# Kernel optimization log

Hardware: AMD Instinct MI355X
Metric: run time of the kernel (lower is better)

## Reference

```python
import jax, jax.numpy as jnp
import numpy as np

EPS = 1e-5  # torch BatchNorm1d default eps


def _bn(x, axes):
    # BatchNorm in training mode with gamma=1, beta=0 (torch init values):
    # normalize with biased batch statistics over the given axes.
    m = x.mean(axes, keepdims=True)
    v = x.var(axes, keepdims=True)
    return (x - m) * jax.lax.rsqrt(v + EPS)


def setup_inputs() -> dict:
    key = jax.random.key(0)
    ks = jax.random.split(key, 12)
    N, M = 50000, 12
    OF, F, E, H = 92, 64, 41, 128
    Z = 2 * F + E  # 169 = concat(node, nbr_node, edge)

    def w(k, shape, fan):
        return jax.random.normal(k, shape, jnp.float32) * np.float32(1.0 / np.sqrt(fan))

    return {
        "node_fea": jax.random.normal(ks[0], (N, OF), jnp.float32),
        "edge_fea": jax.random.uniform(ks[1], (N, M, E), dtype=jnp.float32),
        "nbr_offset": jax.random.randint(ks[2], (N, M, 3), -1, 2).astype(jnp.float32),
        "atom_pos": jax.random.uniform(ks[3], (N, 3), dtype=jnp.float32) * 10.0,
        "cells": jnp.broadcast_to(jnp.eye(3, dtype=jnp.float32) * 10.0, (N, 3, 3))
                 + jax.random.normal(ks[4], (N, 3, 3), jnp.float32) * 0.1,
        "edge_idx": jax.random.randint(ks[5], (N, M), 0, N),
        "W_emb": w(ks[6], (OF, F), OF), "b_emb": jnp.zeros((F,), jnp.float32),
        "W_pre_node": w(ks[7], (3, Z, 2 * F), Z), "b_pre_node": jnp.zeros((3, 2 * F), jnp.float32),
        "W_pre_edge": w(ks[8], (3, Z, 2 * E), Z), "b_pre_edge": jnp.zeros((3, 2 * E), jnp.float32),
        "W_dist": w(ks[9], (Z, H), Z), "b_dist": jnp.zeros((H,), jnp.float32),
        "W_const": w(ks[10], (Z, H), Z), "b_const": jnp.zeros((H,), jnp.float32),
    }


def reference(node_fea, edge_fea, nbr_offset, atom_pos, cells, edge_idx,
              W_emb, b_emb, W_pre_node, b_pre_node, W_pre_edge, b_pre_edge,
              W_dist, b_dist, W_const, b_const):
    N, M = edge_idx.shape
    lrelu = jax.nn.leaky_relu  # torch LeakyReLU default slope 0.01
    sig = jax.nn.sigmoid
    sp = jax.nn.softplus

    # get_distance: neighbor Cartesian positions via unit-cell offsets
    off_cart = jnp.einsum('nmi,nij->nmj', nbr_offset, cells)         # (N,M,3)
    diff = atom_pos[edge_idx] + off_cart - atom_pos[:, None, :]       # (N,M,3)
    distance = jnp.sqrt(jnp.sum(diff * diff, -1, keepdims=True) + 1e-12)  # (N,M,1)

    node = node_fea @ W_emb + b_emb  # embedding -> (N,64)

    for l in range(W_pre_node.shape[0]):  # n_conv = 3 ConvLayers
        nbr = node[edge_idx]  # gather (N,M,F)
        z = jnp.concatenate(
            [jnp.broadcast_to(node[:, None, :], (N, M, node.shape[-1])), nbr, edge_fea],
            axis=2)  # (N,M,169)
        # node branch: linear -> BN -> sigmoid*leakyrelu gate -> sum over M -> BN -> residual
        zn = _bn(z @ W_pre_node[l] + b_pre_node[l], (0, 1))  # (N,M,128)
        nf, nc = jnp.split(zn, 2, axis=2)
        aggr = jnp.sum(sig(nf) * lrelu(nc), axis=1)           # (N,64)
        node = lrelu(node + _bn(aggr, (0,)))
        # edge branch: linear -> BN -> gate -> BN -> residual
        ze = _bn(z @ W_pre_edge[l] + b_pre_edge[l], (0, 1))   # (N,M,82)
        ef, ec = jnp.split(ze, 2, axis=2)
        edge_fea = lrelu(edge_fea + _bn(sig(ef) * lrelu(ec), (0, 1)))

    nbr = node[edge_idx]
    bond_fea = jnp.concatenate(
        [jnp.broadcast_to(node[:, None, :], (N, M, node.shape[-1])), nbr, edge_fea],
        axis=2)  # (N,M,169)

    # n_h_dist == 1 branch: softplus(BN(linear) + distance), mean over channels
    bd = sp(_bn(bond_fea @ W_dist + b_dist, (0, 1)) + distance)
    bd = jnp.mean(bd, axis=2, keepdims=True)                  # (N,M,1)
    # n_h_const == 1 branch: softplus(BN(linear)), mean over channels, / N
    bc = sp(_bn(bond_fea @ W_const + b_const, (0, 1)))
    bc = jnp.mean(bc, axis=2, keepdims=True) / N              # (N,M,1)

    return jnp.concatenate([bd, bc], axis=2)                  # (N,M,2)
```

## Files before the change

kernel.cpp:

```cpp
#include <hip/hip_runtime.h>
#include <math.h>

#define NN 50000
#define MM 12
#define NM 600000
#define OF 92
#define FF 64
#define EE 41
#define ES 48
#define ZZ 169
#define RPB 96
#define NPB 8
#define NTILE 6250
#define NBLK2 3125
#define KP 200
#define KSTEPS 6
#define MT 6
#define NSLICE 64
#define PSTRIDE 1024
#define TPB 512

typedef __bf16 bf16x8 __attribute__((ext_vector_type(8)));
typedef float  f32x4  __attribute__((ext_vector_type(4)));

__device__ __forceinline__ float lrelu(float x){ return fmaxf(x, 0.01f*x); }
__device__ __forceinline__ float sigm(float x){ return __builtin_amdgcn_rcpf(1.f+__expf(-x)); }
__device__ __forceinline__ float softpl(float x){ return fmaxf(x,0.f) + __logf(1.f+__expf(-fabsf(x))); }
__device__ __forceinline__ unsigned short f2bf(float f){
    __bf16 h = (__bf16)f;
    return __builtin_bit_cast(unsigned short, h);
}
__device__ __forceinline__ float b2f(unsigned short u){
    unsigned int b = ((unsigned int)u) << 16;
    return __builtin_bit_cast(float, b);
}

__global__ __launch_bounds__(256) void pack_w(const float* __restrict__ Wn,
    const float* __restrict__ We, const float* __restrict__ Wd,
    const float* __restrict__ Wc, unsigned short* __restrict__ dst)
{
    int idx = blockIdx.x*256 + threadIdx.x;
    if (idx >= 4*49152) return;
    int j    = idx & 7;
    int lane = (idx >> 3) & 63;
    int ntks = (idx >> 9) % 96;
    int L    = idx / 49152;
    int nt = ntks & 15, ks = ntks >> 4;
    int k   = ks*32 + (lane>>4)*8 + j;
    int col = nt*16 + (lane&15);
    float v = 0.f;
    if (k < ZZ) {
        if (L < 3) {
            if (col < 128)                       v = Wn[((size_t)L*ZZ + k)*128 + col];
            else if (col >= 128 && col < 128+EE) v = We[((size_t)L*ZZ + k)*82 + (col-128)];
            else if (col >= 192 && col < 192+EE) v = We[((size_t)L*ZZ + k)*82 + 41 + (col-192)];
        } else {
            if (col < 128) v = Wd[(size_t)k*128 + col];
            else           v = Wc[(size_t)k*128 + (col-128)];
        }
    }
    dst[idx] = f2bf(v);
}

__global__ __launch_bounds__(256) void k_dist(const float* __restrict__ off,
    const float* __restrict__ apos, const float* __restrict__ cells,
    const int* __restrict__ eidx, float* __restrict__ distb)
{
    int idx = blockIdx.x*256 + threadIdx.x;
    if (idx >= NM) return;
    int n = idx / MM;
    const float* o  = off + (size_t)idx*3;
    const float* cl = cells + (size_t)n*9;
    int n2 = eidx[idx];
    float o0=o[0], o1=o[1], o2=o[2];
    float dd = 1e-12f;
    #pragma unroll
    for (int j=0;j<3;j++){
        float oc = o0*cl[0*3+j] + o1*cl[1*3+j] + o2*cl[2*3+j];
        float d = apos[(size_t)n2*3+j] + oc - apos[(size_t)n*3+j];
        dd += d*d;
    }
    distb[idx] = sqrtf(dd);
}

__global__ __launch_bounds__(256) void k_cvt(const float* __restrict__ src,
    unsigned short* __restrict__ e)
{
    int idx = blockIdx.x*256 + threadIdx.x;
    if (idx >= NM*ES) return;
    int gr = idx / ES;
    int c  = idx - gr*ES;
    e[idx] = (c < EE) ? f2bf(src[(size_t)gr*EE + c]) : (unsigned short)0;
}

__global__ __launch_bounds__(256) void k_emb(const float* __restrict__ nf,
    const float* __restrict__ W, const float* __restrict__ b,
    unsigned short* __restrict__ node0)
{
    int idx = blockIdx.x*256 + threadIdx.x;
    if (idx >= NN*FF) return;
    int n = idx >> 6, c = idx & 63;
    float s = b[c];
    for (int k=0;k<OF;k++) s = fmaf(nf[(size_t)n*OF+k], W[k*FF+c], s);
    node0[idx] = f2bf(s);
}

__global__ __launch_bounds__(256) void k_red(float* __restrict__ P,
    float* __restrict__ dst, int lo, int hi)
{
    for (int c = lo + threadIdx.x; c < hi; c += 256) {
        float s = 0.f;
        #pragma unroll 8
        for (int sl = 0; sl < NSLICE; ++sl) s += P[sl*PSTRIDE + c];
        dst[c] = s;
        #pragma unroll 8
        for (int sl = 0; sl < NSLICE; ++sl) P[sl*PSTRIDE + c] = 0.f;
    }
}

__device__ __forceinline__ void stage_load(uint4* __restrict__ R,
    const unsigned short* __restrict__ node_src, const unsigned short* __restrict__ ebuf,
    const unsigned short* __restrict__ gbuf, const int* __restrict__ eidx,
    int n0, int tid, bool upd)
{
    const int gr0 = n0 * MM;
    const int r0 = tid >> 3, ch = tid & 7;
    const bool two = tid < 256;
    const uint4 z4 = make_uint4(0u,0u,0u,0u);
    int e0 = eidx[gr0 + r0];
    R[0] = *(const uint4*)(node_src + (size_t)(n0 + r0/MM)*FF + ch*8);
    R[1] = *(const uint4*)(node_src + (size_t)e0*FF + ch*8);
    R[2] = z4; R[3] = z4; R[4] = z4; R[5] = z4; R[6] = z4; R[7] = z4;
    if (ch < 6) {
        R[2] = *(const uint4*)(ebuf + (size_t)(gr0+r0)*ES + ch*8);
        if (upd) R[3] = *(const uint4*)(gbuf + (size_t)(gr0+r0)*ES + ch*8);
    }
    if (two) {
        int r1 = r0 + 64;
        int e1 = eidx[gr0 + r1];
        R[4] = *(const uint4*)(node_src + (size_t)(n0 + r1/MM)*FF + ch*8);
        R[5] = *(const uint4*)(node_src + (size_t)e1*FF + ch*8);
        if (ch < 6) {
            R[6] = *(const uint4*)(ebuf + (size_t)(gr0+r1)*ES + ch*8);
            if (upd) R[7] = *(const uint4*)(gbuf + (size_t)(gr0+r1)*ES + ch*8);
        }
    }
}

__device__ __forceinline__ uint4 upd_edge8(uint4 e, uint4 g,
    const float* __restrict__ mmv, const float* __restrict__ isv, int ch)
{
    unsigned short es[8], gs[8], os[8];
    *(uint4*)es = e; *(uint4*)gs = g;
    #pragma unroll
    for (int j=0;j<8;j++){
        int c = ch*8+j;
        if (c < EE){
            float v = (b2f(gs[j]) - mmv[j]) * isv[j];
            os[j] = f2bf(lrelu(b2f(es[j]) + v));
        } else os[j] = es[j];
    }
    return *(uint4*)os;
}

__device__ __forceinline__ void stage_write(uint4* __restrict__ R,
    unsigned short* __restrict__ Zl, unsigned short* __restrict__ ebuf_wb,
    int n0, int tid, bool upd,
    const float* __restrict__ mmv, const float* __restrict__ isv)
{
    const int gr0 = n0 * MM;
    const int r0 = tid >> 3, ch = tid & 7;
    const bool two = tid < 256;
    uint4 d0 = R[2];
    if (upd && ch < 6) {
        d0 = upd_edge8(R[2], R[3], mmv, isv, ch);
        *(uint4*)(ebuf_wb + (size_t)(gr0+r0)*ES + ch*8) = d0;
    }
    *(uint4*)(Zl + r0*KP + ch*8)       = R[0];
    *(uint4*)(Zl + r0*KP + 64 + ch*8)  = R[1];
    *(uint4*)(Zl + r0*KP + 128 + ch*8) = d0;
    if (two) {
        int r1 = r0 + 64;
        uint4 d1 = R[6];
        if (upd && ch < 6) {
            d1 = upd_edge8(R[6], R[7], mmv, isv, ch);
            *(uint4*)(ebuf_wb + (size_t)(gr0+r1)*ES + ch*8) = d1;
        }
        *(uint4*)(Zl + r1*KP + ch*8)       = R[4];
        *(uint4*)(Zl + r1*KP + 64 + ch*8)  = R[5];
        *(uint4*)(Zl + r1*KP + 128 + ch*8) = d1;
    }
}

template<bool ZERO>
__device__ __forceinline__ void mfma_core(const unsigned short* __restrict__ Zl,
    const unsigned short* __restrict__ Wpk, int h, int sw, int lane, f32x4 (&acc)[MT][2])
{
    const int quad = lane >> 4, li = lane & 15;
    if (ZERO) {
        #pragma unroll
        for (int mt=0;mt<MT;mt++){
            acc[mt][0] = (f32x4){0.f,0.f,0.f,0.f};
            acc[mt][1] = (f32x4){0.f,0.f,0.f,0.f};
        }
    }
    const int nt0 = h*8 + sw;
    #pragma unroll 2
    for (int ks=0; ks<KSTEPS; ++ks) {
        bf16x8 bfr0 = *(const bf16x8*)(Wpk + (((ks*16 + nt0    )*64 + lane) << 3));
        bf16x8 bfr1 = *(const bf16x8*)(Wpk + (((ks*16 + nt0 + 4)*64 + lane) << 3));
        bf16x8 afr[MT];
        #pragma unroll
        for (int mt=0;mt<MT;mt++)
            afr[mt] = *(const bf16x8*)(Zl + (mt*16+li)*KP + ks*32 + quad*8);
        #pragma unroll
        for (int mt=0;mt<MT;mt++){
            acc[mt][0] = __builtin_amdgcn_mfma_f32_16x16x32_bf16(afr[mt], bfr0, acc[mt][0], 0, 0, 0);
            acc[mt][1] = __builtin_amdgcn_mfma_f32_16x16x32_bf16(afr[mt], bfr1, acc[mt][1], 0, 0, 0);
        }
    }
}

__device__ __forceinline__ void stats_epi(const f32x4 (&acc)[MT][2], int h, int sw, int lane,
    float* __restrict__ Ps)
{
    const int quad = lane>>4, li = lane&15;
    #pragma unroll
    for (int t=0;t<2;t++){
        float s=0.f, q=0.f;
        #pragma unroll
        for (int mt=0;mt<MT;mt++)
            #pragma unroll
            for (int r=0;r<4;r++){ float v = acc[mt][t][r]; s+=v; q = fmaf(v,v,q); }
        s += __shfl_xor(s,16); s += __shfl_xor(s,32);
        q += __shfl_xor(q,16); q += __shfl_xor(q,32);
        if (quad == 0) {
            int col = h*128 + t*64 + sw*16 + li;
            atomicAdd(&Ps[col], s);
            atomicAdd(&Ps[256+col], q);
        }
    }
}

__global__ __launch_bounds__(TPB,3) void k_stats(
    const unsigned short* __restrict__ node_src, unsigned short* __restrict__ ebuf,
    const unsigned short* __restrict__ gbuf, const int* __restrict__ eidx,
    const unsigned short* __restrict__ Wpk,
    const float* __restrict__ gS, const float* __restrict__ gQ,
    float* __restrict__ Pst)
{
    __shared__ unsigned short Zl[RPB*KP];
    const int tid = threadIdx.x, w = tid>>6, lane = tid&63;
    const int h = w>>2, sw = w&3;
    const bool upd = (gS != nullptr);
    const int ch = tid & 7;
    float mmv[8], isv[8];
    if (upd) {
        #pragma unroll
        for (int j=0;j<8;j++){
            int c = ch*8+j;
            float mm = 0.f, is = 0.f;
            if (c < EE) {
                mm = gS[c]*(1.f/(float)NM);
                float vv = gQ[c]*(1.f/(float)NM) - mm*mm;
                is = rsqrtf(vv + 1e-5f);
            }
            mmv[j] = mm; isv[j] = is;
        }
    }
    const int t0 = blockIdx.x * 2;
    uint4 R[8];
    stage_load(R, node_src, ebuf, gbuf, eidx, t0*NPB, tid, upd);
    stage_write(R, Zl, ebuf, t0*NPB, tid, upd, mmv, isv);
    __syncthreads();
    stage_load(R, node_src, ebuf, gbuf, eidx, (t0+1)*NPB, tid, upd);
    f32x4 acc[MT][2];
    mfma_core<true>(Zl, Wpk, h, sw, lane, acc);
    __syncthreads();
    stage_write(R, Zl, ebuf, (t0+1)*NPB, tid, upd, mmv, isv);
    __syncthreads();
    mfma_core<false>(Zl, Wpk, h, sw, lane, acc);
    float* Ps = Pst + (size_t)(blockIdx.x & (NSLICE-1))*PSTRIDE;
    stats_epi(acc, h, sw, lane, Ps);
}

__global__ __launch_bounds__(TPB,3) void k_apply_re(
    const unsigned short* __restrict__ node_src, const unsigned short* __restrict__ ebuf,
    const int* __restrict__ eidx, const unsigned short* __restrict__ Wpk,
    const float* __restrict__ preS, const float* __restrict__ preQ,
    float* __restrict__ aggr, unsigned short* __restrict__ gbuf,
    float* __restrict__ Pst)
{
    __shared__ __align__(16) char smem[RPB*KP*2];
    unsigned short* Zl = (unsigned short*)smem;
    float* gL = (float*)smem;
    const int tid = threadIdx.x, w = tid>>6, lane = tid&63;
    const int quad = lane>>4, li = lane&15;
    const int h = w>>2, sw = w&3;
    const int t0 = blockIdx.x * 2;

    uint4 R[8];
    stage_load(R, node_src, ebuf, nullptr, eidx, t0*NPB, tid, false);
    stage_write(R, Zl, nullptr, t0*NPB, tid, false, nullptr, nullptr);
    __syncthreads();
    stage_load(R, node_src, ebuf, nullptr, eidx, (t0+1)*NPB, tid, false);

    const int cg0 = sw*16 + li;
    float sc[2], bi[2];
    #pragma unroll
    for (int t=0;t<2;t++){
        int col = h*128 + t*64 + cg0;
        float mm = preS[col]*(1.f/(float)NM);
        float vv = preQ[col]*(1.f/(float)NM) - mm*mm;
        float is = rsqrtf(vv + 1e-5f);
        sc[t] = is; bi[t] = -mm*is;
    }
    const bool ce_ok = cg0 < EE;
    float* Ps = Pst + (size_t)(blockIdx.x & (NSLICE-1))*PSTRIDE;
    float pg = 0.f, pq = 0.f;
    float sAcc = 0.f, sQq = 0.f;

    f32x4 acc[MT][2];
    #pragma unroll
    for (int tile=0; tile<2; ++tile){
        const int n0 = (t0+tile)*NPB;
        const int gr0 = n0 * MM;
        mfma_core<true>(Zl, Wpk, h, sw, lane, acc);
        __syncthreads();
        if (h == 0) {
            #pragma unroll
            for (int mt=0;mt<MT;mt++)
                #pragma unroll
                for (int r=0;r<4;r++){
                    int row = mt*16 + quad*4 + r;
                    float nf = fmaf(acc[mt][0][r], sc[0], bi[0]);
                    float nc = fmaf(acc[mt][1][r], sc[1], bi[1]);
                    gL[row*68 + cg0] = sigm(nf) * lrelu(nc);
                }
        } else {
            #pragma unroll
            for (int mt=0;mt<MT;mt++)
                #pragma unroll
                for (int r=0;r<4;r++){
                    int row = mt*16 + quad*4 + r;
                    float ef = fmaf(acc[mt][0][r], sc[0], bi[0]);
                    float ec = fmaf(acc[mt][1][r], sc[1], bi[1]);
                    float gv = sigm(ef)*lrelu(ec);
                    if (ce_ok) {
                        gbuf[(size_t)(gr0+row)*ES + cg0] = f2bf(gv);
                        pg += gv; pq = fmaf(gv,gv,pq);
                    }
                }
        }
        __syncthreads();
        {
            float vsum = 0.f;
            #pragma unroll
            for (int jj=0;jj<MM;jj++) vsum += gL[(w*MM+jj)*68 + lane];
            aggr[(size_t)(n0+w)*64 + lane] = vsum;
            sAcc += vsum; sQq = fmaf(vsum,vsum,sQq);
        }
        if (tile == 0) {
            __syncthreads();
            stage_write(R, Zl, nullptr, (t0+1)*NPB, tid, false, nullptr, nullptr);
            __syncthreads();
        }
    }
    pg += __shfl_xor(pg,16); pg += __shfl_xor(pg,32);
    pq += __shfl_xor(pq,16); pq += __shfl_xor(pq,32);
    if (h==1 && quad==0 && ce_ok){ atomicAdd(&Ps[640+cg0], pg); atomicAdd(&Ps[704+cg0], pq); }
    atomicAdd(&Ps[512+lane], sAcc);
    atomicAdd(&Ps[576+lane], sQq);
}

__global__ __launch_bounds__(256) void k_upd_node(const unsigned short* __restrict__ cur,
    const float* __restrict__ aggr, const float* __restrict__ aS,
    const float* __restrict__ aQ, unsigned short* __restrict__ nxt)
{
    int idx = blockIdx.x*256 + threadIdx.x;
    if (idx >= NN*8) return;
    int n = idx >> 3, ch = idx & 7;
    int base = n*64 + ch*8;
    float4 a0 = *(const float4*)(aggr + base);
    float4 a1 = *(const float4*)(aggr + base + 4);
    uint4 cu = *(const uint4*)(cur + base);
    unsigned short cs[8]; *(uint4*)cs = cu;
    float av[8] = {a0.x,a0.y,a0.z,a0.w,a1.x,a1.y,a1.z,a1.w};
    unsigned short os[8];
    #pragma unroll
    for (int j=0;j<8;j++){
        int c = ch*8+j;
        float mm = aS[c]*(1.f/(float)NN);
        float vv = aQ[c]*(1.f/(float)NN) - mm*mm;
        float is = rsqrtf(vv + 1e-5f);
        float v = (av[j] - mm) * is;
        os[j] = f2bf(lrelu(b2f(cs[j]) + v));
    }
    *(uint4*)(nxt + base) = *(uint4*)os;
}

__global__ __launch_bounds__(TPB,3) void k_final_re(
    const unsigned short* __restrict__ node_src, const unsigned short* __restrict__ ebuf,
    const int* __restrict__ eidx, const unsigned short* __restrict__ Wpk,
    const float* __restrict__ fS, const float* __restrict__ fQ,
    const float* __restrict__ distb, float* __restrict__ out)
{
    __shared__ __align__(16) char smem[RPB*KP*2];
    unsigned short* Zl = (unsigned short*)smem;
    float* bufD = (float*)smem;
    float* bufC = (float*)(smem + 8192);
    const int tid = threadIdx.x, w = tid>>6, lane = tid&63;
    const int quad = lane>>4, li = lane&15;
    const int h = w>>2, sw = w&3;
    const int t0 = blockIdx.x * 2;

    uint4 R[8];
    stage_load(R, node_src, ebuf, nullptr, eidx, t0*NPB, tid, false);
    stage_write(R, Zl, nullptr, t0*NPB, tid, false, nullptr, nullptr);
    __syncthreads();
    stage_load(R, node_src, ebuf, nullptr, eidx, (t0+1)*NPB, tid, false);

    const int cg0 = sw*16 + li;
    float sc[2], bi[2];
    #pragma unroll
    for (int t=0;t<2;t++){
        int col = h*128 + t*64 + cg0;
        float mm = fS[col]*(1.f/(float)NM);
        float vv = fQ[col]*(1.f/(float)NM) - mm*mm;
        float is = rsqrtf(vv + 1e-5f);
        sc[t] = is; bi[t] = -mm*is;
    }
    const int liq = li >> 2;
    const bool wr = (li & 3) == 0;

    f32x4 acc[MT][2];
    #pragma unroll
    for (int tile=0; tile<2; ++tile){
        const int n0 = (t0+tile)*NPB;
        const int gr0 = n0 * MM;
        mfma_core<true>(Zl, Wpk, h, sw, lane, acc);
        __syncthreads();
        float* buf = (h == 0) ? bufD : bufC;
        #pragma unroll
        for (int mt=0;mt<MT;mt++)
            #pragma unroll
            for (int r=0;r<4;r++){
                int row = mt*16 + quad*4 + r;
                float v0 = fmaf(acc[mt][0][r], sc[0], bi[0]);
                float v1 = fmaf(acc[mt][1][r], sc[1], bi[1]);
                float p;
                if (h == 0) {
                    float dv = distb[gr0 + row];
                    p = softpl(v0 + dv) + softpl(v1 + dv);
                } else {
                    p = softpl(v0) + softpl(v1);
                }
                p += __shfl_xor(p,1); p += __shfl_xor(p,2);
                if (wr) buf[row*17 + sw*4 + liq] = p;
            }
        __syncthreads();
        if (tid < 2*RPB) {
            int hh = tid >= RPB;
            int row = tid - (hh ? RPB : 0);
            const float* bsrc = hh ? bufC : bufD;
            float s = 0.f;
            #pragma unroll
            for (int t=0;t<16;t++) s += bsrc[row*17+t];
            size_t gr = gr0 + row;
            out[gr*2 + hh] = hh ? s * (1.f/128.f) * (1.f/(float)NN) : s * (1.f/128.f);
        }
        if (tile == 0) {
            __syncthreads();
            stage_write(R, Zl, nullptr, (t0+1)*NPB, tid, false, nullptr, nullptr);
            __syncthreads();
        }
    }
}

extern "C" void kernel_launch(void* const* d_in, const int* in_sizes, int n_in,
                              void* d_out, int out_size, void* d_ws, size_t ws_size,
                              hipStream_t stream)
{
    const float* node_fea = (const float*)d_in[0];
    const float* edge_in  = (const float*)d_in[1];
    const float* nbr_off  = (const float*)d_in[2];
    const float* apos     = (const float*)d_in[3];
    const float* cells    = (const float*)d_in[4];
    const int*   eidx     = (const int*)  d_in[5];
    const float* W_emb    = (const float*)d_in[6];
    const float* b_emb    = (const float*)d_in[7];
    const float* W_pn     = (const float*)d_in[8];
    const float* W_pe     = (const float*)d_in[10];
    const float* W_dist   = (const float*)d_in[12];
    const float* W_cst    = (const float*)d_in[14];
    float* out = (float*)d_out;
    char* ws = (char*)d_ws;

    size_t o = 0;
    auto alloc = [&](size_t bytes) { char* p = ws + o; o += (bytes + 255) & ~(size_t)255; return p; };
    unsigned short* node0 = (unsigned short*)alloc((size_t)NN*FF*2);
    unsigned short* node1 = (unsigned short*)alloc((size_t)NN*FF*2);
    unsigned short* ebuf  = (unsigned short*)alloc((size_t)NM*ES*2);
    unsigned short* gbuf  = (unsigned short*)alloc((size_t)NM*ES*2);
    float* aggr  = (float*)alloc((size_t)NN*FF*4);
    float* distb = (float*)alloc((size_t)NM*4);
    unsigned short* Wpk = (unsigned short*)alloc((size_t)4*49152*2);
    float* stats = (float*)alloc(4096*4);
    float* Pst   = (float*)alloc((size_t)NSLICE*PSTRIDE*4);

    hipMemsetAsync(stats, 0, 4096*sizeof(float), stream);
    hipMemsetAsync(Pst, 0, (size_t)NSLICE*PSTRIDE*sizeof(float), stream);
    pack_w<<<(4*49152+255)/256, 256, 0, stream>>>(W_pn, W_pe, W_dist, W_cst, Wpk);
    k_dist <<<(NM+255)/256,     256, 0, stream>>>(nbr_off, apos, cells, eidx, distb);
    k_cvt  <<<(NM*ES+255)/256,  256, 0, stream>>>(edge_in, ebuf);
    k_emb  <<<(NN*FF+255)/256,  256, 0, stream>>>(node_fea, W_emb, b_emb, node0);

    const unsigned short* ncur = node0;

    for (int l=0;l<3;l++){
        float* st = stats + l*768;
        float* preS = st;       float* preQ = st+256;
        float* aSs  = st+512;   float* aQq  = st+576;
        const unsigned short* Wl = Wpk + (size_t)l*49152;
        unsigned short* ndst = (l & 1) ? node0 : node1;
        const float* gSp = (l == 0) ? nullptr : (stats + (l-1)*768 + 640);
        const float* gQp = (l == 0) ? nullptr : (stats + (l-1)*768 + 704);

        k_stats  <<<NBLK2,TPB,0,stream>>>(ncur, ebuf, gbuf, eidx, Wl, gSp, gQp, Pst);
        k_red    <<<1,256,0,stream>>>(Pst, st, 0, 512);
        k_apply_re<<<NBLK2,TPB,0,stream>>>(ncur, ebuf, eidx, Wl, preS, preQ,
                                           aggr, gbuf, Pst);
        k_red    <<<1,256,0,stream>>>(Pst, st, 512, 768);
        k_upd_node<<<(NN*8+255)/256,256,0,stream>>>(ncur, aggr, aSs, aQq, ndst);
        ncur = ndst;
    }

    float* fSt = stats + 3*768;
    float* fS = fSt; float* fQ = fSt + 256;
    const unsigned short* Wf = Wpk + (size_t)3*49152;
    const float* gSp = stats + 2*768 + 640;
    const float* gQp = stats + 2*768 + 704;
    k_stats  <<<NBLK2,TPB,0,stream>>>(ncur, ebuf, gbuf, eidx, Wf, gSp, gQp, Pst);
    k_red    <<<1,256,0,stream>>>(Pst, fSt, 0, 512);
    k_final_re<<<NBLK2,TPB,0,stream>>>(ncur, ebuf, eidx, Wf, fS, fQ, distb, out);
}
```

Baseline: 1.380 ms.

## Persistent double-buffered GEMM kernels with direct global-to-LDS loads and swizzled layout

Replaces the two-tiles-per-block launch of the stats/apply/final kernels with a persistent grid of 512 blocks. Each block loops over tiles, double-buffering LDS so the next tile loads while MFMAs run on the current one. Node and neighbour rows are fetched with global_load_lds straight into an XOR-swizzled LDS layout, replacing the padded register-staged copy, and the edge section is staged separately. This aims to hide gather latency and cut LDS bank conflicts, at the cost of twice the LDS per block, more syncs per tile, and stats atomics issued once per tile instead of once per block.

```diff
diff --git a/kernel.cpp b/kernel.cpp
--- a/kernel.cpp
+++ b/kernel.cpp
@@ -12,13 +12,15 @@
 #define RPB 96
 #define NPB 8
 #define NTILE 6250
-#define NBLK2 3125
-#define KP 200
 #define KSTEPS 6
 #define MT 6
 #define NSLICE 64
 #define PSTRIDE 1024
 #define TPB 512
+#define GRIDP 512
+#define ZR0 24576
+#define ZR2 12288
+#define BUFB (ZR0+ZR2)
 
 typedef __bf16 bf16x8 __attribute__((ext_vector_type(8)));
 typedef float  f32x4  __attribute__((ext_vector_type(4)));
@@ -33,6 +35,12 @@
 __device__ __forceinline__ float b2f(unsigned short u){
     unsigned int b = ((unsigned int)u) << 16;
     return __builtin_bit_cast(float, b);
+}
+
+__device__ __forceinline__ void glds16(const void* g, void* l){
+    __builtin_amdgcn_global_load_lds(
+        (const __attribute__((address_space(1))) void*)g,
+        (__attribute__((address_space(3))) void*)l, 16, 0, 0);
 }
 
 __global__ __launch_bounds__(256) void pack_w(const float* __restrict__ Wn,
@@ -118,32 +126,23 @@
     }
 }
 
-__device__ __forceinline__ void stage_load(uint4* __restrict__ R,
-    const unsigned short* __restrict__ node_src, const unsigned short* __restrict__ ebuf,
-    const unsigned short* __restrict__ gbuf, const int* __restrict__ eidx,
-    int n0, int tid, bool upd)
+__device__ __forceinline__ void issue_glds01(char* bufbase,
+    const unsigned short* __restrict__ node_src, const int* __restrict__ eidx,
+    int n0, int w, int lane)
 {
     const int gr0 = n0 * MM;
-    const int r0 = tid >> 3, ch = tid & 7;
-    const bool two = tid < 256;
-    const uint4 z4 = make_uint4(0u,0u,0u,0u);
-    int e0 = eidx[gr0 + r0];
-    R[0] = *(const uint4*)(node_src + (size_t)(n0 + r0/MM)*FF + ch*8);
-    R[1] = *(const uint4*)(node_src + (size_t)e0*FF + ch*8);
-    R[2] = z4; R[3] = z4; R[4] = z4; R[5] = z4; R[6] = z4; R[7] = z4;
-    if (ch < 6) {
-        R[2] = *(const uint4*)(ebuf + (size_t)(gr0+r0)*ES + ch*8);
-        if (upd) R[3] = *(const uint4*)(gbuf + (size_t)(gr0+r0)*ES + ch*8);
-    }
-    if (two) {
-        int r1 = r0 + 64;
-        int e1 = eidx[gr0 + r1];
-        R[4] = *(const uint4*)(node_src + (size_t)(n0 + r1/MM)*FF + ch*8);
-        R[5] = *(const uint4*)(node_src + (size_t)e1*FF + ch*8);
-        if (ch < 6) {
-            R[6] = *(const uint4*)(ebuf + (size_t)(gr0+r1)*ES + ch*8);
-            if (upd) R[7] = *(const uint4*)(gbuf + (size_t)(gr0+r1)*ES + ch*8);
-        }
+    #pragma unroll
+    for (int ii=0; ii<3; ++ii){
+        int i = w + ii*8;
+        int d = i*1024 + lane*16;
+        int r = d >> 8;
+        int c = d & 255;
+        int sec = c >> 7;
+        int ch = (c >> 4) & 7;
+        int k2 = ch ^ (r & 7);
+        int nsrc = n0 + ((r*2731) >> 15);
+        if (sec) nsrc = eidx[gr0 + r];
+        glds16(node_src + (size_t)nsrc*FF + k2*8, bufbase + d);
     }
 }
 
@@ -163,56 +162,54 @@
     return *(uint4*)os;
 }
 
-__device__ __forceinline__ void stage_write(uint4* __restrict__ R,
-    unsigned short* __restrict__ Zl, unsigned short* __restrict__ ebuf_wb,
-    int n0, int tid, bool upd,
+__device__ __forceinline__ void stage_sec2(char* bufbase,
+    const unsigned short* __restrict__ ebuf, const unsigned short* __restrict__ gbuf,
+    unsigned short* __restrict__ ebuf_wb, int n0, int tid, bool upd,
     const float* __restrict__ mmv, const float* __restrict__ isv)
 {
     const int gr0 = n0 * MM;
-    const int r0 = tid >> 3, ch = tid & 7;
-    const bool two = tid < 256;
-    uint4 d0 = R[2];
-    if (upd && ch < 6) {
-        d0 = upd_edge8(R[2], R[3], mmv, isv, ch);
-        *(uint4*)(ebuf_wb + (size_t)(gr0+r0)*ES + ch*8) = d0;
-    }
-    *(uint4*)(Zl + r0*KP + ch*8)       = R[0];
-    *(uint4*)(Zl + r0*KP + 64 + ch*8)  = R[1];
-    *(uint4*)(Zl + r0*KP + 128 + ch*8) = d0;
-    if (two) {
-        int r1 = r0 + 64;
-        uint4 d1 = R[6];
-        if (upd && ch < 6) {
-            d1 = upd_edge8(R[6], R[7], mmv, isv, ch);
-            *(uint4*)(ebuf_wb + (size_t)(gr0+r1)*ES + ch*8) = d1;
-        }
-        *(uint4*)(Zl + r1*KP + ch*8)       = R[4];
-        *(uint4*)(Zl + r1*KP + 64 + ch*8)  = R[5];
-        *(uint4*)(Zl + r1*KP + 128 + ch*8) = d1;
-    }
-}
-
-template<bool ZERO>
-__device__ __forceinline__ void mfma_core(const unsigned short* __restrict__ Zl,
+    unsigned short* Z2 = (unsigned short*)(bufbase + ZR0);
+    for (int task = tid; task < 768; task += TPB) {
+        int r = task >> 3, ch = task & 7;
+        uint4 v = make_uint4(0u,0u,0u,0u);
+        if (ch < 6) {
+            v = *(const uint4*)(ebuf + (size_t)(gr0+r)*ES + ch*8);
+            if (upd) {
+                uint4 g = *(const uint4*)(gbuf + (size_t)(gr0+r)*ES + ch*8);
+                v = upd_edge8(v, g, mmv, isv, ch);
+                *(uint4*)(ebuf_wb + (size_t)(gr0+r)*ES + ch*8) = v;
+            }
+        }
+        *(uint4*)(Z2 + r*64 + ((ch ^ (r&7)) << 3)) = v;
+    }
+}
+
+__device__ __forceinline__ void mfma_core(const char* bufbase,
     const unsigned short* __restrict__ Wpk, int h, int sw, int lane, f32x4 (&acc)[MT][2])
 {
     const int quad = lane >> 4, li = lane & 15;
-    if (ZERO) {
-        #pragma unroll
-        for (int mt=0;mt<MT;mt++){
-            acc[mt][0] = (f32x4){0.f,0.f,0.f,0.f};
-            acc[mt][1] = (f32x4){0.f,0.f,0.f,0.f};
-        }
+    const unsigned short* Z0 = (const unsigned short*)bufbase;
+    const unsigned short* Z2 = (const unsigned short*)(bufbase + ZR0);
+    #pragma unroll
+    for (int mt=0;mt<MT;mt++){
+        acc[mt][0] = (f32x4){0.f,0.f,0.f,0.f};
+        acc[mt][1] = (f32x4){0.f,0.f,0.f,0.f};
     }
     const int nt0 = h*8 + sw;
-    #pragma unroll 2
+    #pragma unroll
     for (int ks=0; ks<KSTEPS; ++ks) {
         bf16x8 bfr0 = *(const bf16x8*)(Wpk + (((ks*16 + nt0    )*64 + lane) << 3));
         bf16x8 bfr1 = *(const bf16x8*)(Wpk + (((ks*16 + nt0 + 4)*64 + lane) << 3));
         bf16x8 afr[MT];
         #pragma unroll
-        for (int mt=0;mt<MT;mt++)
-            afr[mt] = *(const bf16x8*)(Zl + (mt*16+li)*KP + ks*32 + quad*8);
+        for (int mt=0;mt<MT;mt++){
+            int row = mt*16 + li;
+            int x8 = (row & 7) << 3;
+            if (ks < 4)
+                afr[mt] = *(const bf16x8*)(Z0 + row*128 + ((ks*32 + quad*8) ^ x8));
+            else
+                afr[mt] = *(const bf16x8*)(Z2 + row*64  + (((ks-4)*32 + quad*8) ^ x8));
+        }
         #pragma unroll
         for (int mt=0;mt<MT;mt++){
             acc[mt][0] = __builtin_amdgcn_mfma_f32_16x16x32_bf16(afr[mt], bfr0, acc[mt][0], 0, 0, 0);
@@ -242,14 +239,14 @@
     }
 }
 
-__global__ __launch_bounds__(TPB,3) void k_stats(
+__global__ __launch_bounds__(TPB,4) void k_stats(
     const unsigned short* __restrict__ node_src, unsigned short* __restrict__ ebuf,
     const unsigned short* __restrict__ gbuf, const int* __restrict__ eidx,
     const unsigned short* __restrict__ Wpk,
     const float* __restrict__ gS, const float* __restrict__ gQ,
     float* __restrict__ Pst)
 {
-    __shared__ unsigned short Zl[RPB*KP];
+    __shared__ __align__(16) char smem[2*BUFB];
     const int tid = threadIdx.x, w = tid>>6, lane = tid&63;
     const int h = w>>2, sw = w&3;
     const bool upd = (gS != nullptr);
@@ -268,65 +265,69 @@
             mmv[j] = mm; isv[j] = is;
         }
     }
-    const int t0 = blockIdx.x * 2;
-    uint4 R[8];
-    stage_load(R, node_src, ebuf, gbuf, eidx, t0*NPB, tid, upd);
-    stage_write(R, Zl, ebuf, t0*NPB, tid, upd, mmv, isv);
+    float* Ps = Pst + (size_t)(blockIdx.x & (NSLICE-1))*PSTRIDE;
+
+    int t = blockIdx.x, cur = 0;
+    issue_glds01(smem, node_src, eidx, t*NPB, w, lane);
+    stage_sec2(smem, ebuf, gbuf, ebuf, t*NPB, tid, upd, mmv, isv);
+    asm volatile("s_waitcnt vmcnt(0)" ::: "memory");
     __syncthreads();
-    stage_load(R, node_src, ebuf, gbuf, eidx, (t0+1)*NPB, tid, upd);
-    f32x4 acc[MT][2];
-    mfma_core<true>(Zl, Wpk, h, sw, lane, acc);
-    __syncthreads();
-    stage_write(R, Zl, ebuf, (t0+1)*NPB, tid, upd, mmv, isv);
-    __syncthreads();
-    mfma_core<false>(Zl, Wpk, h, sw, lane, acc);
-    float* Ps = Pst + (size_t)(blockIdx.x & (NSLICE-1))*PSTRIDE;
-    stats_epi(acc, h, sw, lane, Ps);
-}
-
-__global__ __launch_bounds__(TPB,3) void k_apply_re(
+    while (t < NTILE) {
+        int tn = t + GRIDP;
+        if (tn < NTILE) {
+            issue_glds01(smem + (cur^1)*BUFB, node_src, eidx, tn*NPB, w, lane);
+            stage_sec2(smem + (cur^1)*BUFB, ebuf, gbuf, ebuf, tn*NPB, tid, upd, mmv, isv);
+        }
+        f32x4 acc[MT][2];
+        mfma_core(smem + cur*BUFB, Wpk, h, sw, lane, acc);
+        stats_epi(acc, h, sw, lane, Ps);
+        asm volatile("s_waitcnt vmcnt(0)" ::: "memory");
+        __syncthreads();
+        cur ^= 1; t = tn;
+    }
+}
+
+__global__ __launch_bounds__(TPB,4) void k_apply_re(
     const unsigned short* __restrict__ node_src, const unsigned short* __restrict__ ebuf,
     const int* __restrict__ eidx, const unsigned short* __restrict__ Wpk,
     const float* __restrict__ preS, const float* __restrict__ preQ,
     float* __restrict__ aggr, unsigned short* __restrict__ gbuf,
     float* __restrict__ Pst)
 {
-    __shared__ __align__(16) char smem[RPB*KP*2];
-    unsigned short* Zl = (unsigned short*)smem;
-    float* gL = (float*)smem;
+    __shared__ __align__(16) char smem[2*BUFB];
     const int tid = threadIdx.x, w = tid>>6, lane = tid&63;
     const int quad = lane>>4, li = lane&15;
     const int h = w>>2, sw = w&3;
-    const int t0 = blockIdx.x * 2;
-
-    uint4 R[8];
-    stage_load(R, node_src, ebuf, nullptr, eidx, t0*NPB, tid, false);
-    stage_write(R, Zl, nullptr, t0*NPB, tid, false, nullptr, nullptr);
-    __syncthreads();
-    stage_load(R, node_src, ebuf, nullptr, eidx, (t0+1)*NPB, tid, false);
-
     const int cg0 = sw*16 + li;
     float sc[2], bi[2];
     #pragma unroll
-    for (int t=0;t<2;t++){
-        int col = h*128 + t*64 + cg0;
+    for (int tt=0;tt<2;tt++){
+        int col = h*128 + tt*64 + cg0;
         float mm = preS[col]*(1.f/(float)NM);
         float vv = preQ[col]*(1.f/(float)NM) - mm*mm;
         float is = rsqrtf(vv + 1e-5f);
-        sc[t] = is; bi[t] = -mm*is;
+        sc[tt] = is; bi[tt] = -mm*is;
     }
     const bool ce_ok = cg0 < EE;
     float* Ps = Pst + (size_t)(blockIdx.x & (NSLICE-1))*PSTRIDE;
-    float pg = 0.f, pq = 0.f;
-    float sAcc = 0.f, sQq = 0.f;
-
-    f32x4 acc[MT][2];
-    #pragma unroll
-    for (int tile=0; tile<2; ++tile){
-        const int n0 = (t0+tile)*NPB;
-        const int gr0 = n0 * MM;
-        mfma_core<true>(Zl, Wpk, h, sw, lane, acc);
-        __syncthreads();
+    float pg = 0.f, pq = 0.f, sAcc = 0.f, sQq = 0.f;
+
+    int t = blockIdx.x, cur = 0;
+    issue_glds01(smem, node_src, eidx, t*NPB, w, lane);
+    stage_sec2(smem, ebuf, nullptr, nullptr, t*NPB, tid, false, nullptr, nullptr);
+    asm volatile("s_waitcnt vmcnt(0)" ::: "memory");
+    __syncthreads();
+    while (t < NTILE) {
+        int tn = t + GRIDP;
+        if (tn < NTILE) {
+            issue_glds01(smem + (cur^1)*BUFB, node_src, eidx, tn*NPB, w, lane);
+            stage_sec2(smem + (cur^1)*BUFB, ebuf, nullptr, nullptr, tn*NPB, tid, false, nullptr, nullptr);
+        }
+        f32x4 acc[MT][2];
+        mfma_core(smem + cur*BUFB, Wpk, h, sw, lane, acc);
+        __syncthreads();
+        float* gL = (float*)(smem + cur*BUFB);
+        const int n0 = t*NPB, gr0 = n0*MM;
         if (h == 0) {
             #pragma unroll
             for (int mt=0;mt<MT;mt++)
@@ -360,11 +361,9 @@
             aggr[(size_t)(n0+w)*64 + lane] = vsum;
             sAcc += vsum; sQq = fmaf(vsum,vsum,sQq);
         }
-        if (tile == 0) {
-            __syncthreads();
-            stage_write(R, Zl, nullptr, (t0+1)*NPB, tid, false, nullptr, nullptr);
-            __syncthreads();
-        }
+        asm volatile("s_waitcnt vmcnt(0)" ::: "memory");
+        __syncthreads();
+        cur ^= 1; t = tn;
     }
     pg += __shfl_xor(pg,16); pg += __shfl_xor(pg,32);
     pq += __shfl_xor(pq,16); pq += __shfl_xor(pq,32);
@@ -399,47 +398,46 @@
     *(uint4*)(nxt + base) = *(uint4*)os;
 }
 
-__global__ __launch_bounds__(TPB,3) void k_final_re(
+__global__ __launch_bounds__(TPB,4) void k_final_re(
     const unsigned short* __restrict__ node_src, const unsigned short* __restrict__ ebuf,
     const int* __restrict__ eidx, const unsigned short* __restrict__ Wpk,
     const float* __restrict__ fS, const float* __restrict__ fQ,
     const float* __restrict__ distb, float* __restrict__ out)
 {
-    __shared__ __align__(16) char smem[RPB*KP*2];
-    unsigned short* Zl = (unsigned short*)smem;
-    float* bufD = (float*)smem;
-    float* bufC = (float*)(smem + 8192);
+    __shared__ __align__(16) char smem[2*BUFB];
     const int tid = threadIdx.x, w = tid>>6, lane = tid&63;
     const int quad = lane>>4, li = lane&15;
     const int h = w>>2, sw = w&3;
-    const int t0 = blockIdx.x * 2;
-
-    uint4 R[8];
-    stage_load(R, node_src, ebuf, nullptr, eidx, t0*NPB, tid, false);
-    stage_write(R, Zl, nullptr, t0*NPB, tid, false, nullptr, nullptr);
-    __syncthreads();
-    stage_load(R, node_src, ebuf, nullptr, eidx, (t0+1)*NPB, tid, false);
-
     const int cg0 = sw*16 + li;
     float sc[2], bi[2];
     #pragma unroll
-    for (int t=0;t<2;t++){
-        int col = h*128 + t*64 + cg0;
+    for (int tt=0;tt<2;tt++){
+        int col = h*128 + tt*64 + cg0;
         float mm = fS[col]*(1.f/(float)NM);
         float vv = fQ[col]*(1.f/(float)NM) - mm*mm;
         float is = rsqrtf(vv + 1e-5f);
-        sc[t] = is; bi[t] = -mm*is;
+        sc[tt] = is; bi[tt] = -mm*is;
     }
     const int liq = li >> 2;
     const bool wr = (li & 3) == 0;
 
-    f32x4 acc[MT][2];
-    #pragma unroll
-    for (int tile=0; tile<2; ++tile){
-        const int n0 = (t0+tile)*NPB;
-        const int gr0 = n0 * MM;
-        mfma_core<true>(Zl, Wpk, h, sw, lane, acc);
-        __syncthreads();
+    int t = blockIdx.x, cur = 0;
+    issue_glds01(smem, node_src, eidx, t*NPB, w, lane);
+    stage_sec2(smem, ebuf, nullptr, nullptr, t*NPB, tid, false, nullptr, nullptr);
+    asm volatile("s_waitcnt vmcnt(0)" ::: "memory");
+    __syncthreads();
+    while (t < NTILE) {
+        int tn = t + GRIDP;
+        if (tn < NTILE) {
+            issue_glds01(smem + (cur^1)*BUFB, node_src, eidx, tn*NPB, w, lane);
+            stage_sec2(smem + (cur^1)*BUFB, ebuf, nullptr, nullptr, tn*NPB, tid, false, nullptr, nullptr);
+        }
+        f32x4 acc[MT][2];
+        mfma_core(smem + cur*BUFB, Wpk, h, sw, lane, acc);
+        __syncthreads();
+        float* bufD = (float*)(smem + cur*BUFB);
+        float* bufC = (float*)(smem + cur*BUFB + 8192);
+        const int n0 = t*NPB, gr0 = n0*MM;
         float* buf = (h == 0) ? bufD : bufC;
         #pragma unroll
         for (int mt=0;mt<MT;mt++)
@@ -465,15 +463,13 @@
             const float* bsrc = hh ? bufC : bufD;
             float s = 0.f;
             #pragma unroll
-            for (int t=0;t<16;t++) s += bsrc[row*17+t];
+            for (int tt=0;tt<16;tt++) s += bsrc[row*17+tt];
             size_t gr = gr0 + row;
             out[gr*2 + hh] = hh ? s * (1.f/128.f) * (1.f/(float)NN) : s * (1.f/128.f);
         }
-        if (tile == 0) {
-            __syncthreads();
-            stage_write(R, Zl, nullptr, (t0+1)*NPB, tid, false, nullptr, nullptr);
-            __syncthreads();
-        }
+        asm volatile("s_waitcnt vmcnt(0)" ::: "memory");
+        __syncthreads();
+        cur ^= 1; t = tn;
     }
 }
 
@@ -526,9 +522,9 @@
         const float* gSp = (l == 0) ? nullptr : (stats + (l-1)*768 + 640);
         const float* gQp = (l == 0) ? nullptr : (stats + (l-1)*768 + 704);
 
-        k_stats  <<<NBLK2,TPB,0,stream>>>(ncur, ebuf, gbuf, eidx, Wl, gSp, gQp, Pst);
+        k_stats  <<<GRIDP,TPB,0,stream>>>(ncur, ebuf, gbuf, eidx, Wl, gSp, gQp, Pst);
         k_red    <<<1,256,0,stream>>>(Pst, st, 0, 512);
-        k_apply_re<<<NBLK2,TPB,0,stream>>>(ncur, ebuf, eidx, Wl, preS, preQ,
+        k_apply_re<<<GRIDP,TPB,0,stream>>>(ncur, ebuf, eidx, Wl, preS, preQ,
                                            aggr, gbuf, Pst);
         k_red    <<<1,256,0,stream>>>(Pst, st, 512, 768);
         k_upd_node<<<(NN*8+255)/256,256,0,stream>>>(ncur, aggr, aSs, aQq, ndst);
@@ -540,7 +536,7 @@
     const unsigned short* Wf = Wpk + (size_t)3*49152;
     const float* gSp = stats + 2*768 + 640;
     const float* gQp = stats + 2*768 + 704;
-    k_stats  <<<NBLK2,TPB,0,stream>>>(ncur, ebuf, gbuf, eidx, Wf, gSp, gQp, Pst);
+    k_stats  <<<GRIDP,TPB,0,stream>>>(ncur, ebuf, gbuf, eidx, Wf, gSp, gQp, Pst);
     k_red    <<<1,256,0,stream>>>(Pst, fSt, 0, 512);
-    k_final_re<<<NBLK2,TPB,0,stream>>>(ncur, ebuf, eidx, Wf, fS, fQ, distb, out);
-}
+    k_final_re<<<GRIDP,TPB,0,stream>>>(ncur, ebuf, eidx, Wf, fS, fQ, distb, out);
+}
```

Measured after the change: 1.744 ms. +26.4%, slower.
